# Optimization experiments

Hardware: AMD Instinct MI355X
Metric: run time of the kernel (lower is better)

## Reference

```python
import jax, jax.numpy as jnp
import numpy as np

B, T, DIM, MDIM, HID = 16, 2048, 1024, 128, 512
WIN = 16
HALF = WIN // 2              # 8 even / 8 odd tokens per window
MAXP = int(0.8 * HALF)       # candidate_ratio * min(nA, nB) = 6 pairs per window
SIM_THRESH = -10.0           # permissive: never masks a cosine similarity
KEEP_RATIO = 0.7
SIM_W, IMP_W, ALPHA_SCALE = 1.0, 0.5, 5.0
LN_EPS = 1e-5


def _ln(x, g, b):
    mu = jnp.mean(x, -1, keepdims=True)
    var = jnp.mean((x - mu) ** 2, -1, keepdims=True)
    return (x - mu) / jnp.sqrt(var + LN_EPS) * g + b


def _greedy(s):
    # s: [HALF, HALF] bipartite sims. Greedy conflict-free matching by descending
    # similarity; since min(nA,nB)=8 >= MAXP=6 it always yields exactly MAXP pairs.
    order = jnp.argsort(-s.reshape(-1))

    def body(k, st):
        usedA, usedB, pa, pb, cnt = st
        idx = order[k]
        iA = (idx // HALF).astype(jnp.int32)
        iB = (idx % HALF).astype(jnp.int32)
        ok = (cnt < MAXP) & (~usedA[iA]) & (~usedB[iB])
        usedA = usedA.at[iA].set(usedA[iA] | ok)
        usedB = usedB.at[iB].set(usedB[iB] | ok)
        w = jnp.where(ok, cnt, MAXP)  # slot MAXP is a scratch slot
        pa = pa.at[w].set(jnp.where(ok, iA, pa[w]))
        pb = pb.at[w].set(jnp.where(ok, iB, pb[w]))
        return (usedA, usedB, pa, pb, cnt + ok.astype(jnp.int32))

    st0 = (jnp.zeros(HALF, bool), jnp.zeros(HALF, bool),
           jnp.zeros(MAXP + 1, jnp.int32), jnp.zeros(MAXP + 1, jnp.int32),
           jnp.int32(0))
    _, _, pa, pb, _ = jax.lax.fori_loop(0, HALF * HALF, body, st0)
    pa, pb = pa[:MAXP], pb[:MAXP]
    return pa, pb, s[pa, pb]


def _forward(x, ln_m_g, ln_m_b, w_match, ln_i_g, ln_i_b, w_imp1, b_imp1, w_imp2, b_imp2):
    Bc, Tc, C = x.shape
    nW = Tc // WIN
    P = nW * MAXP
    K = int((1.0 - KEEP_RATIO) * Tc)  # fixed merge budget (top-K)

    # matching space (L2-normalized) and per-token importance
    m = _ln(x, ln_m_g, ln_m_b) @ w_match                      # [B,T,MDIM]
    m = m / jnp.linalg.norm(m, axis=-1, keepdims=True)
    h = jax.nn.relu(_ln(x, ln_i_g, ln_i_b) @ w_imp1 + b_imp1)
    imp = jax.nn.sigmoid((h @ w_imp2 + b_imp2)[..., 0])       # [B,T]

    # windowed even/odd bipartite similarity
    mw = m.reshape(Bc, nW, WIN, MDIM)
    sim = jnp.einsum('bwad,bwcd->bwac', mw[:, :, 0::2], mw[:, :, 1::2])  # [B,nW,8,8]
    sim = jnp.where(sim < SIM_THRESH, -jnp.inf, sim)

    pa, pb, sv = jax.vmap(jax.vmap(_greedy))(sim)             # [B,nW,MAXP]
    wstart = (jnp.arange(nW, dtype=jnp.int32) * WIN)[None, :, None]
    i_idx = (wstart + 2 * pa).reshape(Bc, P)                  # keep token (even)
    j_idx = (wstart + 2 * pb + 1).reshape(Bc, P)              # drop token (odd)
    sim_c = sv.reshape(Bc, P)
    imp_i = jnp.take_along_axis(imp, i_idx, axis=1)
    imp_j = jnp.take_along_axis(imp, j_idx, axis=1)

    # fixed budget: exactly top-K merges by score (high sim, low importance)
    scores = SIM_W * sim_c - IMP_W * 0.5 * (imp_i + imp_j)
    _, top = jax.lax.top_k(scores, K)
    z = jnp.zeros((Bc, P), x.dtype).at[jnp.arange(Bc)[:, None], top].set(1.0)

    # merge keeps i, drops j; alpha from relative importance
    alpha = jax.nn.sigmoid(ALPHA_SCALE * (imp_i - imp_j))[..., None]
    xi = jnp.take_along_axis(x, i_idx[..., None], axis=1)
    xj = jnp.take_along_axis(x, j_idx[..., None], axis=1)
    merged = alpha * xi + (1.0 - alpha) * xj                  # [B,P,C]

    def pack_one(xb, ib, jb, mb, zb):
        # i indices are globally unique -> scatter merged content where z==1
        x_new = xb.at[ib].add(zb[:, None] * (mb - xb[ib]))
        drop = (jnp.zeros(Tc, xb.dtype).at[jb].add(zb)) > 0.5
        # stable argsort keeps surviving tokens in time order; take first T-K
        order = jnp.argsort(drop.astype(jnp.int32))[:Tc - K]
        return x_new[order]

    return jax.vmap(pack_one)(x, i_idx, j_idx, merged, z)     # [B, T-K, C]


def setup_inputs() -> dict:
    key = jax.random.key(0)
    ks = jax.random.split(key, 4)
    s = 0.02
    return {
        'x': jax.random.normal(ks[0], (B, T, DIM), jnp.float32),
        'ln_m_g': jnp.ones((DIM,), jnp.float32),
        'ln_m_b': jnp.zeros((DIM,), jnp.float32),
        'w_match': jax.random.normal(ks[1], (DIM, MDIM), jnp.float32) * s,
        'ln_i_g': jnp.ones((DIM,), jnp.float32),
        'ln_i_b': jnp.zeros((DIM,), jnp.float32),
        'w_imp1': jax.random.normal(ks[2], (DIM, HID), jnp.float32) * s,
        'b_imp1': jnp.zeros((HID,), jnp.float32),
        'w_imp2': jax.random.normal(ks[3], (HID, 1), jnp.float32) * s,
        'b_imp2': jnp.zeros((1,), jnp.float32),
    }


def reference(x, ln_m_g, ln_m_b, w_match, ln_i_g, ln_i_b, w_imp1, b_imp1, w_imp2, b_imp2):
    return _forward(x, ln_m_g, ln_m_b, w_match, ln_i_g, ln_i_b, w_imp1, b_imp1, w_imp2, b_imp2)
```

## Files before the change

### kernel.cpp

```cpp
#include <hip/hip_runtime.h>
#include <math.h>

#define B_ 16
#define T_ 2048
#define DIM_ 1024
#define MDIM_ 128
#define HID_ 512
#define NCAT 640
#define NW_ 128
#define WINSZ 16
#define MAXP_ 6
#define P_ 768
#define KDROP 614
#define TKEEP 1434
#define NTOK (B_*T_)

typedef unsigned short u16;
typedef __bf16 bf16x8 __attribute__((ext_vector_type(8)));
typedef float f32x4 __attribute__((ext_vector_type(4)));
typedef unsigned short us4 __attribute__((ext_vector_type(4)));

#define OFF_WCAT   0
#define OFF_BIAS   (OFF_WCAT + DIM_*NCAT)
#define OFF_MU     (OFF_BIAS + NCAT)
#define OFF_RS     (OFF_MU + NTOK)
#define OFF_MBUF   (OFF_RS + NTOK)
#define OFF_LOGIT  (OFF_MBUF + NTOK*MDIM_)
#define OFF_IIDX   (OFF_LOGIT + NTOK)
#define OFF_JIDX   (OFF_IIDX + B_*P_)
#define OFF_SV     (OFF_JIDX + B_*P_)
#define OFF_ALPHA  (OFF_SV + B_*P_)
#define OFF_REP    (OFF_ALPHA + B_*P_)
#define OFF_DROP   (OFF_REP + NTOK)
#define OFF_POS    (OFF_DROP + NTOK)

static constexpr size_t F_AH    = 0;
static constexpr size_t F_AL    = F_AH + (size_t)NTOK*DIM_/2;
static constexpr size_t F_BH    = F_AL + (size_t)NTOK*DIM_/2;
static constexpr size_t F_BL    = F_BH + (size_t)NCAT*DIM_/2;
static constexpr size_t F_BIAS  = F_BL + (size_t)NCAT*DIM_/2;
static constexpr size_t F_MBUF  = F_BIAS + NCAT;
static constexpr size_t F_LOGIT = F_MBUF + (size_t)NTOK*MDIM_;
static constexpr size_t F_IIDX  = F_LOGIT + NTOK;
static constexpr size_t F_JIDX  = F_IIDX + (size_t)B_*P_;
static constexpr size_t F_SV    = F_JIDX + (size_t)B_*P_;
static constexpr size_t F_ALPHA = F_SV + (size_t)B_*P_;
static constexpr size_t F_REP   = F_ALPHA + (size_t)B_*P_;
static constexpr size_t F_DROP  = F_REP + NTOK;
static constexpr size_t F_POS   = F_DROP + NTOK;
static constexpr size_t F_TOTAL = F_POS + NTOK;

__device__ __forceinline__ u16 f2bf(float f) {
  unsigned u = __builtin_bit_cast(unsigned, f);
  unsigned r = u + 0x7FFFu + ((u >> 16) & 1u);
  return (u16)(r >> 16);
}
__device__ __forceinline__ float bf2f(u16 h) {
  unsigned u = ((unsigned)h) << 16;
  return __builtin_bit_cast(float, u);
}
__device__ __forceinline__ void gll16(const void* g, void* l) {
  __builtin_amdgcn_global_load_lds((const __attribute__((address_space(1))) void*)g,
                                   (__attribute__((address_space(3))) void*)l, 16, 0, 0);
}


__global__ __launch_bounds__(256) void prep_a(const float* __restrict__ x,
    u16* __restrict__ Ah, u16* __restrict__ Al) {
  int token = blockIdx.x * 4 + (threadIdx.x >> 6);
  int lane = threadIdx.x & 63;
  const float4* xr = (const float4*)(x + (size_t)token * DIM_);
  float4 v[4];
  float sum = 0.f;
#pragma unroll
  for (int it = 0; it < 4; ++it) {
    v[it] = xr[lane + it * 64];
    sum += v[it].x + v[it].y + v[it].z + v[it].w;
  }
  for (int o = 32; o > 0; o >>= 1) sum += __shfl_xor(sum, o);
  float m = sum * (1.f / 1024.f);
  float ss = 0.f;
#pragma unroll
  for (int it = 0; it < 4; ++it) {
    float a = v[it].x - m, b = v[it].y - m, c = v[it].z - m, d = v[it].w - m;
    ss += a * a + b * b + c * c + d * d;
  }
  for (int o = 32; o > 0; o >>= 1) ss += __shfl_xor(ss, o);
  float rsv = 1.0f / sqrtf(ss * (1.f / 1024.f) + 1e-5f);
#pragma unroll
  for (int it = 0; it < 4; ++it) {
    float e[4] = {(v[it].x - m) * rsv, (v[it].y - m) * rsv,
                  (v[it].z - m) * rsv, (v[it].w - m) * rsv};
    us4 hv, lv;
#pragma unroll
    for (int j = 0; j < 4; ++j) {
      u16 h = f2bf(e[j]);
      hv[j] = h;
      lv[j] = f2bf(e[j] - bf2f(h));
    }
    size_t off = (size_t)token * DIM_ + (size_t)(lane + it * 64) * 4;
    *(us4*)&Ah[off] = hv;
    *(us4*)&Al[off] = lv;
  }
}

__global__ __launch_bounds__(256) void prep_w(const float* __restrict__ wm,
    const float* __restrict__ wi, const float* __restrict__ gm,
    const float* __restrict__ gi, const float* __restrict__ bm,
    const float* __restrict__ bi, const float* __restrict__ b1,
    u16* __restrict__ Bh, u16* __restrict__ Bl, float* __restrict__ biascat) {
  int bid = blockIdx.x;
  const int NBLK_B = (NCAT * DIM_) / 256;
  if (bid < NBLK_B) {
    int e = bid * 256 + threadIdx.x;
    int n = e >> 10, k = e & 1023;
    float wv = (n < MDIM_) ? gm[k] * wm[k * MDIM_ + n]
                           : gi[k] * wi[k * HID_ + (n - MDIM_)];
    u16 h = f2bf(wv);
    Bh[e] = h;
    Bl[e] = f2bf(wv - bf2f(h));
  } else {
    int c = bid - NBLK_B;
    float s = 0.f;
    for (int k = threadIdx.x; k < DIM_; k += 256)
      s += (c < MDIM_) ? bm[k] * wm[k * MDIM_ + c]
                       : bi[k] * wi[k * HID_ + (c - MDIM_)];
    __shared__ float red[256];
    red[threadIdx.x] = s; __syncthreads();
    for (int o = 128; o > 0; o >>= 1) {
      if (threadIdx.x < o) red[threadIdx.x] += red[threadIdx.x + o];
      __syncthreads();
    }
    if (threadIdx.x == 0)
      biascat[c] = red[0] + ((c >= MDIM_) ? b1[c - MDIM_] : 0.f);
  }
}

__global__ __launch_bounds__(256, 2) void gemm_mfma(
    const u16* __restrict__ Ah, const u16* __restrict__ Al,
    const u16* __restrict__ Bh, const u16* __restrict__ Bl,
    const float* __restrict__ biascat, const float* __restrict__ w2,
    float* __restrict__ mbuf, float* __restrict__ logit) {
  __shared__ __align__(16) u16 sAH[2][8 * 512];
  __shared__ __align__(16) u16 sAL[2][8 * 512];
  __shared__ __align__(16) u16 sBH[2][8 * 512];
  __shared__ __align__(16) u16 sBL[2][8 * 512];
  const int tid = threadIdx.x;
  const int w = tid >> 6, lane = tid & 63;
  int bid = blockIdx.x;
  int q = bid / 40, rem = bid % 40;
  int ct = rem >> 3, x8 = rem & 7;
  int stripe = x8 + 8 * q;
  const int row0 = stripe * 128, col0 = ct * 128;
  const int wy = w >> 1, wx = w & 1;
  const int m16 = lane & 15, quad = lane >> 4;

  const u16* gA = (w == 0) ? Ah : (w == 1) ? Al : (w == 2) ? Bh : Bl;
  u16* lds0 = ((w == 0) ? sAH[0] : (w == 1) ? sAL[0] : (w == 2) ? sBH[0] : sBL[0]) + lane * 8;
  u16* lds1 = ((w == 0) ? sAH[1] : (w == 1) ? sAL[1] : (w == 2) ? sBH[1] : sBL[1]) + lane * 8;
  const int rbase = (w < 2) ? row0 : col0;
  const u16* gsrc0 = gA + (size_t)(rbase + m16) * DIM_ + quad * 8;

#pragma unroll
  for (int t = 0; t < 8; ++t)
    gll16(gsrc0 + (size_t)t * 16 * DIM_, lds0 + t * 512);

  f32x4 acc[4][4] = {};
  for (int k0 = 0; k0 < 32; ++k0) {
    __syncthreads();
    if (k0 + 1 < 32) {
      u16* nb = (k0 & 1) ? lds0 : lds1;
#pragma unroll
      for (int t = 0; t < 8; ++t)
        gll16(gsrc0 + (size_t)t * 16 * DIM_ + (k0 + 1) * 32, nb + t * 512);
    }
    const int cb = k0 & 1;
    bf16x8 ah[4], al[4], bh[4], bl[4];
#pragma unroll
    for (int i = 0; i < 4; ++i) {
      ah[i] = *(const bf16x8*)&sAH[cb][(wy * 4 + i) * 512 + lane * 8];
      al[i] = *(const bf16x8*)&sAL[cb][(wy * 4 + i) * 512 + lane * 8];
      bh[i] = *(const bf16x8*)&sBH[cb][(wx * 4 + i) * 512 + lane * 8];
      bl[i] = *(const bf16x8*)&sBL[cb][(wx * 4 + i) * 512 + lane * 8];
    }
#pragma unroll
    for (int i = 0; i < 4; ++i)
#pragma unroll
      for (int j = 0; j < 4; ++j) {
        acc[i][j] = __builtin_amdgcn_mfma_f32_16x16x32_bf16(ah[i], bh[j], acc[i][j], 0, 0, 0);
        acc[i][j] = __builtin_amdgcn_mfma_f32_16x16x32_bf16(ah[i], bl[j], acc[i][j], 0, 0, 0);
        acc[i][j] = __builtin_amdgcn_mfma_f32_16x16x32_bf16(al[i], bh[j], acc[i][j], 0, 0, 0);
      }
  }
  if (ct == 0) {
#pragma unroll
    for (int i = 0; i < 4; ++i)
#pragma unroll
      for (int j = 0; j < 4; ++j) {
        int col = wx * 64 + j * 16 + m16;
        float bs = biascat[col];
#pragma unroll
        for (int r = 0; r < 4; ++r) {
          int row = row0 + wy * 64 + i * 16 + quad * 4 + r;
          mbuf[(size_t)row * MDIM_ + col] = acc[i][j][r] + bs;
        }
      }
  } else {
#pragma unroll
    for (int i = 0; i < 4; ++i) {
      float part[4] = {0.f, 0.f, 0.f, 0.f};
#pragma unroll
      for (int j = 0; j < 4; ++j) {
        int col = col0 + wx * 64 + j * 16 + m16;
        float bs = biascat[col];
        float wv = w2[col - MDIM_];
#pragma unroll
        for (int r = 0; r < 4; ++r) {
          float v = acc[i][j][r] + bs;
          v = v > 0.f ? v : 0.f;
          part[r] += v * wv;
        }
      }
#pragma unroll
      for (int r = 0; r < 4; ++r) {
        part[r] += __shfl_xor(part[r], 1);
        part[r] += __shfl_xor(part[r], 2);
        part[r] += __shfl_xor(part[r], 4);
        part[r] += __shfl_xor(part[r], 8);
      }
      if (m16 == 0)
#pragma unroll
        for (int r = 0; r < 4; ++r)
          atomicAdd(&logit[row0 + wy * 64 + i * 16 + quad * 4 + r], part[r]);
    }
  }
}


__global__ __launch_bounds__(256) void simgreedy(const float* __restrict__ mbuf,
    int* __restrict__ ii, int* __restrict__ jj, float* __restrict__ sv) {
  __shared__ __align__(16) float sm[4][16][132];
  int wv = threadIdx.x >> 6, lane = threadIdx.x & 63;
  int win = blockIdx.x * 4 + wv;
  int b = win >> 7, w = win & 127;
  size_t base = ((size_t)b * T_ + w * WINSZ) * MDIM_;
#pragma unroll
  for (int it = 0; it < 8; ++it) {
    int e4 = it * 64 + lane;
    int row = e4 >> 5, c4 = e4 & 31;
    float4 v = *(const float4*)(mbuf + base + (size_t)row * MDIM_ + c4 * 4);
    *(float4*)&sm[wv][row][c4 * 4] = v;
  }
  __syncthreads();
  {
    int row = lane >> 2, seg = lane & 3;
    float* r = sm[wv][row] + seg * 32;
    float ss = 0.f;
#pragma unroll
    for (int k = 0; k < 32; ++k) ss += r[k] * r[k];
    ss += __shfl_xor(ss, 1);
    ss += __shfl_xor(ss, 2);
    float inv = 1.0f / sqrtf(ss);
#pragma unroll
    for (int k = 0; k < 32; ++k) r[k] *= inv;
  }
  __syncthreads();
  int a = lane >> 3, c = lane & 7;
  const float* ev = sm[wv][2 * a];
  const float* od = sm[wv][2 * c + 1];
  float s = 0.f;
#pragma unroll
  for (int k = 0; k < MDIM_; ++k) s += ev[k] * od[k];
  if (s < -10.0f) s = -__builtin_inff();
  float v = s;
  bool alive = true;
  int outb = (b * NW_ + w) * MAXP_;
  for (int p = 0; p < MAXP_; ++p) {
    float bv = alive ? v : -__builtin_inff();
    int bi = lane;
    for (int o = 32; o > 0; o >>= 1) {
      float ov = __shfl_xor(bv, o);
      int oi = __shfl_xor(bi, o);
      if (ov > bv || (ov == bv && oi < bi)) { bv = ov; bi = oi; }
    }
    int wa = bi >> 3, wc = bi & 7;
    if (lane == 0) {
      ii[outb + p] = w * WINSZ + 2 * wa;
      jj[outb + p] = w * WINSZ + 2 * wc + 1;
      sv[outb + p] = bv;
    }
    if (a == wa || c == wc) alive = false;
  }
}

__global__ __launch_bounds__(256) void select_fused(const float* __restrict__ sv,
    const int* __restrict__ ii, const int* __restrict__ jj,
    const float* __restrict__ logit, const float* __restrict__ b2,
    float* __restrict__ alpha, int* __restrict__ rep,
    int* __restrict__ drop, int* __restrict__ pos) {
  int b = blockIdx.x, tid = threadIdx.x;
  __shared__ float sc[P_];
  __shared__ int sdrop[T_];
  __shared__ int wtot[4];
  float bb = b2[0];
  for (int t = tid; t < T_; t += 256) {
    sdrop[t] = 0;
    rep[b * T_ + t] = -1;
  }
  for (int p = tid; p < P_; p += 256) {
    int i = ii[b * P_ + p], j = jj[b * P_ + p];
    float fi = 1.f / (1.f + expf(-(logit[b * T_ + i] + bb)));
    float fj = 1.f / (1.f + expf(-(logit[b * T_ + j] + bb)));
    sc[p] = sv[b * P_ + p] - 0.25f * (fi + fj);
    alpha[b * P_ + p] = 1.f / (1.f + expf(-5.f * (fi - fj)));
  }
  __syncthreads();
  for (int p = tid; p < P_; p += 256) {
    float s = sc[p];
    int cnt = 0;
    for (int q = 0; q < P_; ++q) {
      float t = sc[q];
      cnt += (t > s) || (t == s && q < p);
    }
    if (cnt < KDROP) {
      rep[b * T_ + ii[b * P_ + p]] = p;
      sdrop[jj[b * P_ + p]] = 1;
    }
  }
  __syncthreads();
  int base = tid * 8;
  int loc[8];
  int s = 0;
#pragma unroll
  for (int k = 0; k < 8; ++k) { loc[k] = s; s += (sdrop[base + k] ? 0 : 1); }
  int lane = tid & 63, wvi = tid >> 6;
  int incl = s;
  for (int o = 1; o < 64; o <<= 1) {
    int n = __shfl_up(incl, o);
    if (lane >= o) incl += n;
  }
  if (lane == 63) wtot[wvi] = incl;
  __syncthreads();
  int carry = 0;
  for (int ww = 0; ww < wvi; ++ww) carry += wtot[ww];
  int excl = carry + incl - s;
#pragma unroll
  for (int k = 0; k < 8; ++k) {
    int t = base + k;
    drop[b * T_ + t] = sdrop[t];
    pos[b * T_ + t] = excl + loc[k];
  }
}

__global__ __launch_bounds__(256) void pack_kernel(const float* __restrict__ x,
    const int* __restrict__ drop, const int* __restrict__ pos,
    const int* __restrict__ rep, const float* __restrict__ alpha,
    const int* __restrict__ jj, float* __restrict__ out) {
  int t = blockIdx.x, b = blockIdx.y;
  if (drop[b * T_ + t]) return;
  int tid = threadIdx.x;
  const float4* xi = (const float4*)(x + ((size_t)b * T_ + t) * DIM_);
  float4 v = xi[tid];
  int p = rep[b * T_ + t];
  if (p >= 0) {
    float a = alpha[b * P_ + p];
    int j = jj[b * P_ + p];
    const float4* xj = (const float4*)(x + ((size_t)b * T_ + j) * DIM_);
    float4 vj = xj[tid];
    v.x = a * v.x + (1.f - a) * vj.x;
    v.y = a * v.y + (1.f - a) * vj.y;
    v.z = a * v.z + (1.f - a) * vj.z;
    v.w = a * v.w + (1.f - a) * vj.w;
  }
  int np = pos[b * T_ + t];
  ((float4*)(out + ((size_t)b * TKEEP + np) * DIM_))[tid] = v;
}


__global__ __launch_bounds__(256) void build_wcat(const float* __restrict__ wm,
    const float* __restrict__ wi, const float* __restrict__ gm,
    const float* __restrict__ gi, float* __restrict__ Wcat) {
  int e = blockIdx.x * 256 + threadIdx.x;
  if (e >= DIM_ * NCAT) return;
  int k = e / NCAT, c = e - k * NCAT;
  float v = (c < MDIM_) ? gm[k] * wm[k * MDIM_ + c]
                        : gi[k] * wi[k * HID_ + (c - MDIM_)];
  Wcat[e] = v;
}

__global__ __launch_bounds__(256) void build_bias(const float* __restrict__ wm,
    const float* __restrict__ wi, const float* __restrict__ bm,
    const float* __restrict__ bi, const float* __restrict__ b1,
    float* __restrict__ biascat) {
  int c = blockIdx.x;
  float s = 0.f;
  for (int k = threadIdx.x; k < DIM_; k += 256)
    s += (c < MDIM_) ? bm[k] * wm[k * MDIM_ + c]
                     : bi[k] * wi[k * HID_ + (c - MDIM_)];
  __shared__ float red[256];
  red[threadIdx.x] = s; __syncthreads();
  for (int o = 128; o > 0; o >>= 1) {
    if (threadIdx.x < o) red[threadIdx.x] += red[threadIdx.x + o];
    __syncthreads();
  }
  if (threadIdx.x == 0)
    biascat[c] = red[0] + ((c >= MDIM_) ? b1[c - MDIM_] : 0.f);
}

__global__ __launch_bounds__(256) void ln_stats(const float* __restrict__ x,
    float* __restrict__ mu, float* __restrict__ rs) {
  int token = blockIdx.x * 4 + (threadIdx.x >> 6);
  int lane = threadIdx.x & 63;
  const float4* xr = (const float4*)(x + (size_t)token * DIM_);
  float4 v[4];
  float sum = 0.f;
#pragma unroll
  for (int it = 0; it < 4; ++it) {
    v[it] = xr[lane + it * 64];
    sum += v[it].x + v[it].y + v[it].z + v[it].w;
  }
  for (int o = 32; o > 0; o >>= 1) sum += __shfl_xor(sum, o);
  float m = sum * (1.f / 1024.f);
  float ss = 0.f;
#pragma unroll
  for (int it = 0; it < 4; ++it) {
    float a = v[it].x - m, b = v[it].y - m, c = v[it].z - m, d = v[it].w - m;
    ss += a * a + b * b + c * c + d * d;
  }
  for (int o = 32; o > 0; o >>= 1) ss += __shfl_xor(ss, o);
  if (lane == 0) {
    mu[token] = m;
    rs[token] = 1.0f / sqrtf(ss * (1.f / 1024.f) + 1e-5f);
  }
}

__global__ __launch_bounds__(256) void gemm640(const float* __restrict__ x,
    const float* __restrict__ mu, const float* __restrict__ rs,
    const float* __restrict__ Wcat, const float* __restrict__ biascat,
    const float* __restrict__ w2, float* __restrict__ mbuf,
    float* __restrict__ logit) {
  __shared__ __align__(16) float As[16][68];
  __shared__ __align__(16) float Bs[16][68];
  const int tid = threadIdx.x;
  const int row0 = blockIdx.x * 64, col0 = blockIdx.y * 64;
  const int tx = tid & 15, ty = tid >> 4;
  const int arow = tid >> 2, akk = (tid & 3) << 2;
  const int brow = tid >> 4, bnn = (tid & 15) << 2;
  const int t_g = row0 + arow;
  const float tmu = mu[t_g], trs = rs[t_g];
  const float* xrow = x + (size_t)t_g * DIM_ + akk;
  const float* wptr = Wcat + (size_t)brow * NCAT + col0 + bnn;
  float acc[4][4] = {};
  for (int k0 = 0; k0 < DIM_; k0 += 16) {
    float4 av = *(const float4*)(xrow + k0);
    float4 bv = *(const float4*)(wptr + (size_t)k0 * NCAT);
    As[akk + 0][arow] = (av.x - tmu) * trs;
    As[akk + 1][arow] = (av.y - tmu) * trs;
    As[akk + 2][arow] = (av.z - tmu) * trs;
    As[akk + 3][arow] = (av.w - tmu) * trs;
    *(float4*)&Bs[brow][bnn] = bv;
    __syncthreads();
#pragma unroll
    for (int k = 0; k < 16; ++k) {
      float4 a = *(const float4*)&As[k][ty << 2];
      float4 b = *(const float4*)&Bs[k][tx << 2];
      acc[0][0] += a.x * b.x; acc[0][1] += a.x * b.y; acc[0][2] += a.x * b.z; acc[0][3] += a.x * b.w;
      acc[1][0] += a.y * b.x; acc[1][1] += a.y * b.y; acc[1][2] += a.y * b.z; acc[1][3] += a.y * b.w;
      acc[2][0] += a.z * b.x; acc[2][1] += a.z * b.y; acc[2][2] += a.z * b.z; acc[2][3] += a.z * b.w;
      acc[3][0] += a.w * b.x; acc[3][1] += a.w * b.y; acc[3][2] += a.w * b.z; acc[3][3] += a.w * b.w;
    }
    __syncthreads();
  }
  float bias[4];
#pragma unroll
  for (int j = 0; j < 4; ++j) bias[j] = biascat[col0 + (tx << 2) + j];
  if (col0 < MDIM_) {
#pragma unroll
    for (int i = 0; i < 4; ++i) {
      int t = row0 + (ty << 2) + i;
      float4 o;
      o.x = acc[i][0] + bias[0]; o.y = acc[i][1] + bias[1];
      o.z = acc[i][2] + bias[2]; o.w = acc[i][3] + bias[3];
      *(float4*)(mbuf + (size_t)t * MDIM_ + col0 + (tx << 2)) = o;
    }
  } else {
    float w2v[4];
#pragma unroll
    for (int j = 0; j < 4; ++j) w2v[j] = w2[col0 - MDIM_ + (tx << 2) + j];
#pragma unroll
    for (int i = 0; i < 4; ++i) {
      float p = 0.f;
#pragma unroll
      for (int j = 0; j < 4; ++j) {
        float v = acc[i][j] + bias[j];
        v = v > 0.f ? v : 0.f;
        p += v * w2v[j];
      }
      p += __shfl_xor(p, 1); p += __shfl_xor(p, 2);
      p += __shfl_xor(p, 4); p += __shfl_xor(p, 8);
      if (tx == 0) atomicAdd(&logit[row0 + (ty << 2) + i], p);
    }
  }
}

extern "C" void kernel_launch(void* const* d_in, const int* in_sizes, int n_in,
                              void* d_out, int out_size, void* d_ws, size_t ws_size,
                              hipStream_t stream) {
  const float* x    = (const float*)d_in[0];
  const float* gm   = (const float*)d_in[1];
  const float* bm   = (const float*)d_in[2];
  const float* wm   = (const float*)d_in[3];
  const float* gi   = (const float*)d_in[4];
  const float* bi   = (const float*)d_in[5];
  const float* wi   = (const float*)d_in[6];
  const float* b1   = (const float*)d_in[7];
  const float* w2   = (const float*)d_in[8];
  const float* b2   = (const float*)d_in[9];
  float* ws = (float*)d_ws;
  float* out = (float*)d_out;

  if (ws_size >= F_TOTAL * sizeof(float)) {
    u16* Ah = (u16*)(ws + F_AH);
    u16* Al = (u16*)(ws + F_AL);
    u16* Bh = (u16*)(ws + F_BH);
    u16* Bl = (u16*)(ws + F_BL);
    float* bias  = ws + F_BIAS;
    float* mbuf  = ws + F_MBUF;
    float* logit = ws + F_LOGIT;
    int* iidx    = (int*)(ws + F_IIDX);
    int* jidx    = (int*)(ws + F_JIDX);
    float* sv    = ws + F_SV;
    float* alpha = ws + F_ALPHA;
    int* rep     = (int*)(ws + F_REP);
    int* drop    = (int*)(ws + F_DROP);
    int* pos     = (int*)(ws + F_POS);

    hipMemsetAsync(logit, 0, NTOK * sizeof(float), stream);
    prep_w<<<(NCAT * DIM_) / 256 + NCAT, 256, 0, stream>>>(wm, wi, gm, gi, bm, bi, b1, Bh, Bl, bias);
    prep_a<<<NTOK / 4, 256, 0, stream>>>(x, Ah, Al);
    gemm_mfma<<<(NTOK / 128) * (NCAT / 128), 256, 0, stream>>>(Ah, Al, Bh, Bl, bias, w2, mbuf, logit);
    simgreedy<<<(B_ * NW_) / 4, 256, 0, stream>>>(mbuf, iidx, jidx, sv);
    select_fused<<<B_, 256, 0, stream>>>(sv, iidx, jidx, logit, b2, alpha, rep, drop, pos);
    dim3 pgrid(T_, B_);
    pack_kernel<<<pgrid, 256, 0, stream>>>(x, drop, pos, rep, alpha, jidx, out);
  } else {
    float* Wcat = ws + OFF_WCAT;
    float* bias = ws + OFF_BIAS;
    float* mu   = ws + OFF_MU;
    float* rs   = ws + OFF_RS;
    float* mbuf = ws + OFF_MBUF;
    float* logit = ws + OFF_LOGIT;
    int* iidx   = (int*)(ws + OFF_IIDX);
    int* jidx   = (int*)(ws + OFF_JIDX);
    float* sv   = ws + OFF_SV;
    float* alpha = ws + OFF_ALPHA;
    int* rep    = (int*)(ws + OFF_REP);
    int* drop   = (int*)(ws + OFF_DROP);
    int* pos    = (int*)(ws + OFF_POS);

    hipMemsetAsync(logit, 0, NTOK * sizeof(float), stream);
    build_wcat<<<(DIM_ * NCAT + 255) / 256, 256, 0, stream>>>(wm, wi, gm, gi, Wcat);
    build_bias<<<NCAT, 256, 0, stream>>>(wm, wi, bm, bi, b1, bias);
    ln_stats<<<NTOK / 4, 256, 0, stream>>>(x, mu, rs);
    dim3 ggrid(NTOK / 64, NCAT / 64);
    gemm640<<<ggrid, 256, 0, stream>>>(x, mu, rs, Wcat, bias, w2, mbuf, logit);
    simgreedy<<<(B_ * NW_) / 4, 256, 0, stream>>>(mbuf, iidx, jidx, sv);
    select_fused<<<B_, 256, 0, stream>>>(sv, iidx, jidx, logit, b2, alpha, rep, drop, pos);
    dim3 pgrid(T_, B_);
    pack_kernel<<<pgrid, 256, 0, stream>>>(x, drop, pos, rep, alpha, jidx, out);
  }
}
```

Measured before the change: 530.5 us.

## Load GEMM B operand directly to registers, fold logit zeroing, batch pack tokens

The MFMA GEMM no longer stages the B (weight) hi/lo tiles through LDS. Each wave loads its B fragments straight from global memory into registers every k-step, and only A goes through the double-buffered LDS. Halving LDS use allows the occupancy hint to rise to 3 blocks per CU. The logit memset is folded into prep_a, and pack_kernel now handles 8 tokens per block to cut block count. The risks are higher global-load latency on the B path and more register pressure at the higher occupancy target.

```diff
diff --git a/kernel.cpp b/kernel.cpp
--- a/kernel.cpp
+++ b/kernel.cpp
@@ -66,9 +66,10 @@
 
 
 __global__ __launch_bounds__(256) void prep_a(const float* __restrict__ x,
-    u16* __restrict__ Ah, u16* __restrict__ Al) {
+    u16* __restrict__ Ah, u16* __restrict__ Al, float* __restrict__ logit) {
   int token = blockIdx.x * 4 + (threadIdx.x >> 6);
   int lane = threadIdx.x & 63;
+  if (lane == 0) logit[token] = 0.f;
   const float4* xr = (const float4*)(x + (size_t)token * DIM_);
   float4 v[4];
   float sum = 0.f;
@@ -136,15 +137,13 @@
   }
 }
 
-__global__ __launch_bounds__(256, 2) void gemm_mfma(
+__global__ __launch_bounds__(256, 3) void gemm_mfma(
     const u16* __restrict__ Ah, const u16* __restrict__ Al,
     const u16* __restrict__ Bh, const u16* __restrict__ Bl,
     const float* __restrict__ biascat, const float* __restrict__ w2,
     float* __restrict__ mbuf, float* __restrict__ logit) {
   __shared__ __align__(16) u16 sAH[2][8 * 512];
   __shared__ __align__(16) u16 sAL[2][8 * 512];
-  __shared__ __align__(16) u16 sBH[2][8 * 512];
-  __shared__ __align__(16) u16 sBL[2][8 * 512];
   const int tid = threadIdx.x;
   const int w = tid >> 6, lane = tid & 63;
   int bid = blockIdx.x;
@@ -155,42 +154,68 @@
   const int wy = w >> 1, wx = w & 1;
   const int m16 = lane & 15, quad = lane >> 4;
 
-  const u16* gA = (w == 0) ? Ah : (w == 1) ? Al : (w == 2) ? Bh : Bl;
-  u16* lds0 = ((w == 0) ? sAH[0] : (w == 1) ? sAL[0] : (w == 2) ? sBH[0] : sBL[0]) + lane * 8;
-  u16* lds1 = ((w == 0) ? sAH[1] : (w == 1) ? sAL[1] : (w == 2) ? sBH[1] : sBL[1]) + lane * 8;
-  const int rbase = (w < 2) ? row0 : col0;
-  const u16* gsrc0 = gA + (size_t)(rbase + m16) * DIM_ + quad * 8;
-
-#pragma unroll
-  for (int t = 0; t < 8; ++t)
-    gll16(gsrc0 + (size_t)t * 16 * DIM_, lds0 + t * 512);
+  const u16* gA = (w < 2) ? Ah : Al;
+  const int th = (w & 1) * 4;
+  const u16* gsrcA = gA + (size_t)(row0 + th * 16 + m16) * DIM_ + quad * 8;
+  u16* ldsA0 = ((w < 2) ? sAH[0] : sAL[0]) + th * 512 + lane * 8;
+  u16* ldsA1 = ((w < 2) ? sAH[1] : sAL[1]) + th * 512 + lane * 8;
+
+  const size_t nb0 = (size_t)(col0 + wx * 64 + m16) * DIM_ + (size_t)(quad * 8);
+  const u16* pbh0 = Bh + nb0;
+  const u16* pbh1 = pbh0 + 16 * DIM_;
+  const u16* pbh2 = pbh0 + 32 * DIM_;
+  const u16* pbh3 = pbh0 + 48 * DIM_;
+  const u16* pbl0 = Bl + nb0;
+  const u16* pbl1 = pbl0 + 16 * DIM_;
+  const u16* pbl2 = pbl0 + 32 * DIM_;
+  const u16* pbl3 = pbl0 + 48 * DIM_;
+
+#pragma unroll
+  for (int t = 0; t < 4; ++t)
+    gll16(gsrcA + (size_t)t * 16 * DIM_, ldsA0 + t * 512);
 
   f32x4 acc[4][4] = {};
   for (int k0 = 0; k0 < 32; ++k0) {
     __syncthreads();
+    bf16x8 bh0 = *(const bf16x8*)pbh0;
+    bf16x8 bh1 = *(const bf16x8*)pbh1;
+    bf16x8 bh2 = *(const bf16x8*)pbh2;
+    bf16x8 bh3 = *(const bf16x8*)pbh3;
+    bf16x8 bl0 = *(const bf16x8*)pbl0;
+    bf16x8 bl1 = *(const bf16x8*)pbl1;
+    bf16x8 bl2 = *(const bf16x8*)pbl2;
+    bf16x8 bl3 = *(const bf16x8*)pbl3;
+    __builtin_amdgcn_sched_barrier(0);
     if (k0 + 1 < 32) {
-      u16* nb = (k0 & 1) ? lds0 : lds1;
-#pragma unroll
-      for (int t = 0; t < 8; ++t)
-        gll16(gsrc0 + (size_t)t * 16 * DIM_ + (k0 + 1) * 32, nb + t * 512);
+      u16* nb = (k0 & 1) ? ldsA0 : ldsA1;
+#pragma unroll
+      for (int t = 0; t < 4; ++t)
+        gll16(gsrcA + (size_t)t * 16 * DIM_ + (k0 + 1) * 32, nb + t * 512);
     }
     const int cb = k0 & 1;
-    bf16x8 ah[4], al[4], bh[4], bl[4];
+    bf16x8 ah[4], al[4];
 #pragma unroll
     for (int i = 0; i < 4; ++i) {
       ah[i] = *(const bf16x8*)&sAH[cb][(wy * 4 + i) * 512 + lane * 8];
       al[i] = *(const bf16x8*)&sAL[cb][(wy * 4 + i) * 512 + lane * 8];
-      bh[i] = *(const bf16x8*)&sBH[cb][(wx * 4 + i) * 512 + lane * 8];
-      bl[i] = *(const bf16x8*)&sBL[cb][(wx * 4 + i) * 512 + lane * 8];
-    }
-#pragma unroll
-    for (int i = 0; i < 4; ++i)
-#pragma unroll
-      for (int j = 0; j < 4; ++j) {
-        acc[i][j] = __builtin_amdgcn_mfma_f32_16x16x32_bf16(ah[i], bh[j], acc[i][j], 0, 0, 0);
-        acc[i][j] = __builtin_amdgcn_mfma_f32_16x16x32_bf16(ah[i], bl[j], acc[i][j], 0, 0, 0);
-        acc[i][j] = __builtin_amdgcn_mfma_f32_16x16x32_bf16(al[i], bh[j], acc[i][j], 0, 0, 0);
-      }
+    }
+#pragma unroll
+    for (int i = 0; i < 4; ++i) {
+      acc[i][0] = __builtin_amdgcn_mfma_f32_16x16x32_bf16(ah[i], bh0, acc[i][0], 0, 0, 0);
+      acc[i][1] = __builtin_amdgcn_mfma_f32_16x16x32_bf16(ah[i], bh1, acc[i][1], 0, 0, 0);
+      acc[i][2] = __builtin_amdgcn_mfma_f32_16x16x32_bf16(ah[i], bh2, acc[i][2], 0, 0, 0);
+      acc[i][3] = __builtin_amdgcn_mfma_f32_16x16x32_bf16(ah[i], bh3, acc[i][3], 0, 0, 0);
+      acc[i][0] = __builtin_amdgcn_mfma_f32_16x16x32_bf16(ah[i], bl0, acc[i][0], 0, 0, 0);
+      acc[i][1] = __builtin_amdgcn_mfma_f32_16x16x32_bf16(ah[i], bl1, acc[i][1], 0, 0, 0);
+      acc[i][2] = __builtin_amdgcn_mfma_f32_16x16x32_bf16(ah[i], bl2, acc[i][2], 0, 0, 0);
+      acc[i][3] = __builtin_amdgcn_mfma_f32_16x16x32_bf16(ah[i], bl3, acc[i][3], 0, 0, 0);
+      acc[i][0] = __builtin_amdgcn_mfma_f32_16x16x32_bf16(al[i], bh0, acc[i][0], 0, 0, 0);
+      acc[i][1] = __builtin_amdgcn_mfma_f32_16x16x32_bf16(al[i], bh1, acc[i][1], 0, 0, 0);
+      acc[i][2] = __builtin_amdgcn_mfma_f32_16x16x32_bf16(al[i], bh2, acc[i][2], 0, 0, 0);
+      acc[i][3] = __builtin_amdgcn_mfma_f32_16x16x32_bf16(al[i], bh3, acc[i][3], 0, 0, 0);
+    }
+    pbh0 += 32; pbh1 += 32; pbh2 += 32; pbh3 += 32;
+    pbl0 += 32; pbl1 += 32; pbl2 += 32; pbl3 += 32;
   }
   if (ct == 0) {
 #pragma unroll
@@ -356,24 +381,30 @@
     const int* __restrict__ drop, const int* __restrict__ pos,
     const int* __restrict__ rep, const float* __restrict__ alpha,
     const int* __restrict__ jj, float* __restrict__ out) {
-  int t = blockIdx.x, b = blockIdx.y;
-  if (drop[b * T_ + t]) return;
+  int b = blockIdx.y;
+  int t0 = blockIdx.x * 8;
   int tid = threadIdx.x;
-  const float4* xi = (const float4*)(x + ((size_t)b * T_ + t) * DIM_);
-  float4 v = xi[tid];
-  int p = rep[b * T_ + t];
-  if (p >= 0) {
-    float a = alpha[b * P_ + p];
-    int j = jj[b * P_ + p];
-    const float4* xj = (const float4*)(x + ((size_t)b * T_ + j) * DIM_);
-    float4 vj = xj[tid];
-    v.x = a * v.x + (1.f - a) * vj.x;
-    v.y = a * v.y + (1.f - a) * vj.y;
-    v.z = a * v.z + (1.f - a) * vj.z;
-    v.w = a * v.w + (1.f - a) * vj.w;
-  }
-  int np = pos[b * T_ + t];
-  ((float4*)(out + ((size_t)b * TKEEP + np) * DIM_))[tid] = v;
+  const int bT = b * T_;
+#pragma unroll 1
+  for (int tt = 0; tt < 8; ++tt) {
+    int t = t0 + tt;
+    if (drop[bT + t]) continue;
+    const float4* xi = (const float4*)(x + ((size_t)bT + t) * DIM_);
+    float4 v = xi[tid];
+    int p = rep[bT + t];
+    if (p >= 0) {
+      float a = alpha[b * P_ + p];
+      int j = jj[b * P_ + p];
+      const float4* xj = (const float4*)(x + ((size_t)bT + j) * DIM_);
+      float4 vj = xj[tid];
+      v.x = a * v.x + (1.f - a) * vj.x;
+      v.y = a * v.y + (1.f - a) * vj.y;
+      v.z = a * v.z + (1.f - a) * vj.z;
+      v.w = a * v.w + (1.f - a) * vj.w;
+    }
+    int np = pos[bT + t];
+    ((float4*)(out + ((size_t)b * TKEEP + np) * DIM_))[tid] = v;
+  }
 }
 
 
@@ -535,13 +566,12 @@
     int* drop    = (int*)(ws + F_DROP);
     int* pos     = (int*)(ws + F_POS);
 
-    hipMemsetAsync(logit, 0, NTOK * sizeof(float), stream);
     prep_w<<<(NCAT * DIM_) / 256 + NCAT, 256, 0, stream>>>(wm, wi, gm, gi, bm, bi, b1, Bh, Bl, bias);
-    prep_a<<<NTOK / 4, 256, 0, stream>>>(x, Ah, Al);
+    prep_a<<<NTOK / 4, 256, 0, stream>>>(x, Ah, Al, logit);
     gemm_mfma<<<(NTOK / 128) * (NCAT / 128), 256, 0, stream>>>(Ah, Al, Bh, Bl, bias, w2, mbuf, logit);
     simgreedy<<<(B_ * NW_) / 4, 256, 0, stream>>>(mbuf, iidx, jidx, sv);
     select_fused<<<B_, 256, 0, stream>>>(sv, iidx, jidx, logit, b2, alpha, rep, drop, pos);
-    dim3 pgrid(T_, B_);
+    dim3 pgrid(T_ / 8, B_);
     pack_kernel<<<pgrid, 256, 0, stream>>>(x, drop, pos, rep, alpha, jidx, out);
   } else {
     float* Wcat = ws + OFF_WCAT;
@@ -566,7 +596,7 @@
     gemm640<<<ggrid, 256, 0, stream>>>(x, mu, rs, Wcat, bias, w2, mbuf, logit);
     simgreedy<<<(B_ * NW_) / 4, 256, 0, stream>>>(mbuf, iidx, jidx, sv);
     select_fused<<<B_, 256, 0, stream>>>(sv, iidx, jidx, logit, b2, alpha, rep, drop, pos);
-    dim3 pgrid(T_, B_);
+    dim3 pgrid(T_ / 8, B_);
     pack_kernel<<<pgrid, 256, 0, stream>>>(x, drop, pos, rep, alpha, jidx, out);
   }
 }
```

New measurement: 584.3 us. 1.1x slower.
